# Performance work log

Hardware: AMD Instinct MI355X
Metric: run time of the kernel (lower is better)

The kernel has to match this reference:

```python
import jax, jax.numpy as jnp
import numpy as np

B, N, D, E, H = 16, 256, 64, 64, 8


def setup_inputs() -> dict:
    key = jax.random.key(0)
    ks = jax.random.split(key, 16)
    s = 0.05
    return {
        "query": jax.random.normal(ks[0], (B, N, D), jnp.float32),
        "edges_augmented": jax.random.normal(ks[1], (B, N, N, E), jnp.float32),
        "Wq": jax.random.normal(ks[2], (D, H * D), jnp.float32) * s,
        "bq": jnp.zeros((H * D,), jnp.float32),
        "Wk": jax.random.normal(ks[3], (D, H * D), jnp.float32) * s,
        "bk": jnp.zeros((H * D,), jnp.float32),
        "Wv": jax.random.normal(ks[4], (D, H * D), jnp.float32) * s,
        "bv": jnp.zeros((H * D,), jnp.float32),
        "Wa": jax.random.normal(ks[5], (E, H), jnp.float32) * s,
        "ba": jnp.zeros((H,), jnp.float32),
        "Wg": jax.random.normal(ks[6], (E, H), jnp.float32) * s,
        "bg": jnp.zeros((H,), jnp.float32),
        "Wo": jax.random.normal(ks[7], (H * D, D), jnp.float32) * s,
        "bo": jnp.zeros((D,), jnp.float32),
        "We": jax.random.normal(ks[8], (H, E), jnp.float32) * s,
        "be": jnp.zeros((E,), jnp.float32),
    }


def reference(query, edges_augmented, Wq, bq, Wk, bk, Wv, bv, Wa, ba, Wg, bg, Wo, bo, We, be):
    b, n, d = query.shape
    h = Wa.shape[1]
    # QKV projections -> [b, h, n, d]
    Q = (query @ Wq + bq).reshape(b, n, h, d).transpose(0, 2, 1, 3)
    Kt = (query @ Wk + bk).reshape(b, n, h, d).transpose(0, 2, 1, 3)
    V = (query @ Wv + bv).reshape(b, n, h, d).transpose(0, 2, 1, 3)
    scores = jnp.einsum('bhnd,bhmd->bhnm', Q, Kt) / jnp.sqrt(jnp.asarray(d, query.dtype))
    # edge-derived additive bias: [b,n,n,h] -> [b,h,n,n]
    attn_bias = (edges_augmented @ Wa + ba).transpose(0, 3, 1, 2)
    scores = scores + attn_bias
    # sigmoid gate on values
    g = jax.nn.sigmoid((edges_augmented @ Wg + bg).transpose(0, 3, 1, 2))  # [b,h,n,n]
    Vg = jnp.einsum('bhnm,bhmd->bhnd', g, V)
    attn = jax.nn.softmax(scores, axis=-1)
    out = jnp.einsum('bhnm,bhmd->bhnd', attn, Vg)
    out = out.transpose(0, 2, 1, 3).reshape(b, n, h * d)
    attention_output = out @ Wo + bo  # [b, n, d]
    # edges output: scores [b,h,n,m] -> [b,m,n,h] -> Dense to E
    edges_output = scores.transpose(0, 3, 2, 1) @ We + be  # [b, n, n, E]
    return (attention_output, edges_output)
```

## Files before the change

kernel.cpp:

```cpp
#include <hip/hip_runtime.h>

#define BB 16
#define NN 256
#define DD 64
#define EE 64
#define HH 8

typedef __attribute__((ext_vector_type(4))) float f32x4;
typedef __attribute__((ext_vector_type(8))) short short8;

__device__ __forceinline__ void fma4(float* acc, float x, float4 w) {
    acc[0] += x * w.x; acc[1] += x * w.y; acc[2] += x * w.z; acc[3] += x * w.w;
}

__device__ __forceinline__ unsigned short f2bf(float f) {
    union { float f; unsigned u; } v; v.f = f;
    unsigned r = v.u + 0x7FFFu + ((v.u >> 16) & 1u);
    return (unsigned short)(r >> 16);
}

__global__ __launch_bounds__(256) void qkv_kernel(
    const float* __restrict__ query,
    const float* __restrict__ Wq, const float* __restrict__ bq,
    const float* __restrict__ Wk, const float* __restrict__ bk,
    const float* __restrict__ Wv, const float* __restrict__ bv,
    unsigned short* __restrict__ Qb, unsigned short* __restrict__ Kb,
    unsigned short* __restrict__ Vtb)
{
    __shared__ __align__(16) float q_l[8][64];
    const int mtx = blockIdx.x >> 9;
    const int rem = blockIdx.x & 511;
    const int b   = rem >> 5;
    const int n0  = (rem & 31) << 3;
    const int tid = threadIdx.x;

    if (tid < 128)
        ((float4*)&q_l[0][0])[tid] =
            ((const float4*)(query + (size_t)(b * NN + n0) * DD))[tid];

    const int w    = tid >> 6;
    const int lane = tid & 63;
    const int r0   = w * 2;
    const float* W  = (mtx == 0) ? Wq : (mtx == 1) ? Wk : Wv;
    const float* bs = (mtx == 0) ? bq : (mtx == 1) ? bk : bv;

    const int c0 = lane << 2;
    float acc[2][2][4];
    {
        const float4 b0 = *(const float4*)(bs + c0);
        const float4 b1 = *(const float4*)(bs + 256 + c0);
        acc[0][0][0]=b0.x; acc[0][0][1]=b0.y; acc[0][0][2]=b0.z; acc[0][0][3]=b0.w;
        acc[0][1][0]=b1.x; acc[0][1][1]=b1.y; acc[0][1][2]=b1.z; acc[0][1][3]=b1.w;
        acc[1][0][0]=b0.x; acc[1][0][1]=b0.y; acc[1][0][2]=b0.z; acc[1][0][3]=b0.w;
        acc[1][1][0]=b1.x; acc[1][1][1]=b1.y; acc[1][1][2]=b1.z; acc[1][1][3]=b1.w;
    }
    __syncthreads();

    #pragma unroll 2
    for (int d4 = 0; d4 < 16; ++d4) {
        const float4 qa = ((const float4*)&q_l[r0][0])[d4];
        const float4 qb = ((const float4*)&q_l[r0 + 1][0])[d4];
        const float qav[4] = {qa.x, qa.y, qa.z, qa.w};
        const float qbv[4] = {qb.x, qb.y, qb.z, qb.w};
        #pragma unroll
        for (int k = 0; k < 4; ++k) {
            const float4 w0 = *(const float4*)(W + (size_t)(d4 * 4 + k) * 512 + c0);
            const float4 w1 = *(const float4*)(W + (size_t)(d4 * 4 + k) * 512 + 256 + c0);
            fma4(acc[0][0], qav[k], w0); fma4(acc[0][1], qav[k], w1);
            fma4(acc[1][0], qbv[k], w0); fma4(acc[1][1], qbv[k], w1);
        }
    }

    const int hq = lane >> 4;
    const int d0 = (lane & 15) << 2;
    if (mtx < 2) {
        unsigned short* T = (mtx == 0) ? Qb : Kb;
        const float scale = (mtx == 0) ? 0.125f : 1.0f;
        #pragma unroll
        for (int r = 0; r < 2; ++r)
            #pragma unroll
            for (int j = 0; j < 2; ++j) {
                const int h = j * 4 + hq;
                const unsigned int lo = (unsigned)f2bf(acc[r][j][0] * scale)
                                      | ((unsigned)f2bf(acc[r][j][1] * scale) << 16);
                const unsigned int hi = (unsigned)f2bf(acc[r][j][2] * scale)
                                      | ((unsigned)f2bf(acc[r][j][3] * scale) << 16);
                uint2* p = (uint2*)(T + ((size_t)(b * HH + h) * NN + n0 + r0 + r) * DD + d0);
                *p = make_uint2(lo, hi);
            }
    } else {
        #pragma unroll
        for (int r = 0; r < 2; ++r)
            #pragma unroll
            for (int j = 0; j < 2; ++j) {
                const int h = j * 4 + hq;
                #pragma unroll
                for (int k = 0; k < 4; ++k)
                    Vtb[((size_t)(b * HH + h) * DD + d0 + k) * NN + n0 + r0 + r] =
                        f2bf(acc[r][j][k]);
            }
    }
}

__global__ __launch_bounds__(256) void qk_kernel(
    const unsigned short* __restrict__ Qb, const unsigned short* __restrict__ Kb,
    float* __restrict__ scores)
{
    const int bh = blockIdx.x >> 3;
    const int nt = (blockIdx.x >> 1) & 3;
    const int mh = blockIdx.x & 1;
    const int tid = threadIdx.x;
    const int w = tid >> 6, l = tid & 63;
    const int lr = l & 15, lg = l >> 4;
    const int n0 = nt * 64 + w * 16;

    const unsigned short* qp = Qb + ((size_t)bh * NN + n0 + lr) * DD + lg * 8;
    const unsigned short* kp = Kb + ((size_t)bh * NN + mh * 128 + lr) * DD + lg * 8;

    const short8 a0 = *(const short8*)qp;
    const short8 a1 = *(const short8*)(qp + 32);

    f32x4 acc[8];
    #pragma unroll
    for (int mt = 0; mt < 8; ++mt) acc[mt] = (f32x4){0.f, 0.f, 0.f, 0.f};

    #pragma unroll
    for (int mt = 0; mt < 8; ++mt) {
        const short8 b0 = *(const short8*)(kp + (size_t)mt * 16 * DD);
        const short8 b1 = *(const short8*)(kp + (size_t)mt * 16 * DD + 32);
        acc[mt] = __builtin_amdgcn_mfma_f32_16x16x32_bf16(a0, b0, acc[mt], 0, 0, 0);
        acc[mt] = __builtin_amdgcn_mfma_f32_16x16x32_bf16(a1, b1, acc[mt], 0, 0, 0);
    }

    float* sp = scores + (size_t)bh * NN * NN;
    #pragma unroll
    for (int mt = 0; mt < 8; ++mt)
        #pragma unroll
        for (int r = 0; r < 4; ++r)
            sp[(size_t)(n0 + lg * 4 + r) * NN + mh * 128 + mt * 16 + lr] = acc[mt][r];
}

__global__ __launch_bounds__(256) void edges_kernel(
    const float* __restrict__ edges,
    const float* __restrict__ Wa, const float* __restrict__ ba,
    const float* __restrict__ Wg, const float* __restrict__ bg,
    const float* __restrict__ We, const float* __restrict__ be,
    float* __restrict__ scores,
    unsigned short* __restrict__ gates,
    float* __restrict__ edges_out)
{
    __shared__ __align__(16) float wa_l[EE * HH];
    __shared__ __align__(16) float wg_l[EE * HH];
    __shared__ float ba_l[HH], bg_l[HH];
    __shared__ __align__(16) float sc_l[4][64][HH];

    const int mt   = blockIdx.x & 3;
    const int nt   = (blockIdx.x >> 2) & 63;
    const int b    = blockIdx.x >> 8;
    const int n0   = nt << 2;
    const int m0   = mt << 6;
    const int tid  = threadIdx.x;
    const int lane = tid & 63;
    const int np   = tid >> 6;
    const int mp   = lane;

    for (int i = tid; i < 512; i += 256) { wa_l[i] = Wa[i]; wg_l[i] = Wg[i]; }
    if (tid < 8) { ba_l[tid] = ba[tid]; bg_l[tid] = bg[tid]; }

    float wecol[8];
    #pragma unroll
    for (int h = 0; h < 8; ++h) wecol[h] = We[h * EE + lane];
    const float bev = be[lane];

    const size_t so = (size_t)b * HH * NN * NN + (size_t)(n0 + np) * NN + m0 + mp;
    float qk[8];
    #pragma unroll
    for (int h = 0; h < 8; ++h) qk[h] = scores[so + (size_t)h * NN * NN];

    const float4* ep = (const float4*)(edges +
                        (size_t)((b * NN + n0 + np) * NN + m0 + mp) * DD);
    float4 xr[16];
    #pragma unroll
    for (int i = 0; i < 16; ++i) xr[i] = ep[i];

    __syncthreads();

    float bias[8], gate[8];
    #pragma unroll
    for (int h = 0; h < 8; ++h) { bias[h] = ba_l[h]; gate[h] = bg_l[h]; }
    #pragma unroll
    for (int e4 = 0; e4 < 16; ++e4) {
        const float xs[4] = {xr[e4].x, xr[e4].y, xr[e4].z, xr[e4].w};
        #pragma unroll
        for (int k = 0; k < 4; ++k) {
            const int e = e4 * 4 + k;
            const float4 wa0 = *(const float4*)&wa_l[e * 8];
            const float4 wa1 = *(const float4*)&wa_l[e * 8 + 4];
            const float4 wg0 = *(const float4*)&wg_l[e * 8];
            const float4 wg1 = *(const float4*)&wg_l[e * 8 + 4];
            fma4(&bias[0], xs[k], wa0); fma4(&bias[4], xs[k], wa1);
            fma4(&gate[0], xs[k], wg0); fma4(&gate[4], xs[k], wg1);
        }
    }

    float sc[8];
    #pragma unroll
    for (int h = 0; h < 8; ++h) {
        sc[h] = qk[h] + bias[h];
        const float gg = 1.f / (1.f + __expf(-gate[h]));
        scores[so + (size_t)h * NN * NN] = sc[h];
        gates [so + (size_t)h * NN * NN] = f2bf(gg);
    }
    *(float4*)&sc_l[np][mp][0] = make_float4(sc[0], sc[1], sc[2], sc[3]);
    *(float4*)&sc_l[np][mp][4] = make_float4(sc[4], sc[5], sc[6], sc[7]);
    __syncthreads();

    #pragma unroll 8
    for (int pi = 0; pi < 64; ++pi) {
        const int p   = np * 64 + pi;
        const int mp2 = p >> 2, np2 = p & 3;
        const float4 sa = *(const float4*)&sc_l[np2][mp2][0];
        const float4 sb = *(const float4*)&sc_l[np2][mp2][4];
        const float v = bev
            + sa.x * wecol[0] + sa.y * wecol[1] + sa.z * wecol[2] + sa.w * wecol[3]
            + sb.x * wecol[4] + sb.y * wecol[5] + sb.z * wecol[6] + sb.w * wecol[7];
        edges_out[(size_t)((b * NN + m0 + mp2) * NN + n0 + np2) * DD + lane] = v;
    }
}

__global__ __launch_bounds__(256) void vg_kernel(
    const unsigned short* __restrict__ gates, const unsigned short* __restrict__ Vtb,
    unsigned short* __restrict__ Vgt)
{
    const int bh = blockIdx.x >> 2;
    const int q  = blockIdx.x & 3;
    const int tid = threadIdx.x;
    const int w = tid >> 6, l = tid & 63;
    const int lr = l & 15, lg = l >> 4;
    const int n0 = q * 64 + w * 16;

    const unsigned short* gp = gates + ((size_t)bh * NN + n0 + lr) * NN + lg * 8;
    const unsigned short* vp = Vtb + ((size_t)bh * DD + lr) * NN + lg * 8;

    f32x4 acc[4];
    #pragma unroll
    for (int dt = 0; dt < 4; ++dt) acc[dt] = (f32x4){0.f, 0.f, 0.f, 0.f};

    #pragma unroll
    for (int ks = 0; ks < 8; ++ks) {
        const short8 bfr = *(const short8*)(gp + ks * 32);
        #pragma unroll
        for (int dt = 0; dt < 4; ++dt) {
            const short8 afr = *(const short8*)(vp + (size_t)dt * 16 * NN + ks * 32);
            acc[dt] = __builtin_amdgcn_mfma_f32_16x16x32_bf16(afr, bfr, acc[dt], 0, 0, 0);
        }
    }

    unsigned short* op = Vgt + (size_t)bh * DD * NN;
    #pragma unroll
    for (int dt = 0; dt < 4; ++dt)
        #pragma unroll
        for (int r = 0; r < 4; ++r)
            op[(size_t)(dt * 16 + lg * 4 + r) * NN + n0 + lr] = f2bf(acc[dt][r]);
}

__global__ __launch_bounds__(256) void out_kernel(
    const float* __restrict__ scores, const unsigned short* __restrict__ Vgt,
    const float* __restrict__ Wo, const float* __restrict__ bo,
    float* __restrict__ att_out)
{
    __shared__ __align__(16) float o_l[16][513];
    const int b  = blockIdx.x >> 4;
    const int nt = blockIdx.x & 15;
    const int n0 = nt * 16;
    const int tid = threadIdx.x;
    const int w = tid >> 6, l = tid & 63;
    const int lr = l & 15, lg = l >> 4;

    #pragma unroll
    for (int hw = 0; hw < 2; ++hw) {
        const int h = w + hw * 4;
        const float* sp = scores + ((size_t)(b * HH + h) * NN + n0 + lr) * NN + lg * 8;

        float s[64];
        #pragma unroll
        for (int ks = 0; ks < 8; ++ks) {
            const float4 x0 = *(const float4*)(sp + ks * 32);
            const float4 x1 = *(const float4*)(sp + ks * 32 + 4);
            s[ks * 8 + 0] = x0.x; s[ks * 8 + 1] = x0.y;
            s[ks * 8 + 2] = x0.z; s[ks * 8 + 3] = x0.w;
            s[ks * 8 + 4] = x1.x; s[ks * 8 + 5] = x1.y;
            s[ks * 8 + 6] = x1.z; s[ks * 8 + 7] = x1.w;
        }
        float mx = -1e30f;
        #pragma unroll
        for (int i = 0; i < 64; ++i) mx = fmaxf(mx, s[i]);
        mx = fmaxf(mx, __shfl_xor(mx, 16, 64));
        mx = fmaxf(mx, __shfl_xor(mx, 32, 64));
        float sm = 0.f;
        #pragma unroll
        for (int i = 0; i < 64; ++i) { s[i] = __expf(s[i] - mx); sm += s[i]; }
        sm += __shfl_xor(sm, 16, 64);
        sm += __shfl_xor(sm, 32, 64);
        const float inv = 1.f / sm;

        const unsigned short* vp = Vgt + ((size_t)(b * HH + h) * DD + lr) * NN + lg * 8;
        f32x4 acc[4];
        #pragma unroll
        for (int dt = 0; dt < 4; ++dt) acc[dt] = (f32x4){0.f, 0.f, 0.f, 0.f};

        #pragma unroll
        for (int ks = 0; ks < 8; ++ks) {
            union { short8 v; unsigned short u[8]; } bf;
            #pragma unroll
            for (int j = 0; j < 8; ++j) bf.u[j] = f2bf(s[ks * 8 + j] * inv);
            #pragma unroll
            for (int dt = 0; dt < 4; ++dt) {
                const short8 afr = *(const short8*)(vp + (size_t)dt * 16 * NN + ks * 32);
                acc[dt] = __builtin_amdgcn_mfma_f32_16x16x32_bf16(afr, bf.v, acc[dt], 0, 0, 0);
            }
        }
        #pragma unroll
        for (int dt = 0; dt < 4; ++dt)
            #pragma unroll
            for (int r = 0; r < 4; ++r)
                o_l[lr][h * 64 + dt * 16 + lg * 4 + r] = acc[dt][r];
    }
    __syncthreads();

    const int n  = tid >> 4;
    const int d4 = (tid & 15) << 2;
    float a0 = bo[d4], a1 = bo[d4 + 1], a2 = bo[d4 + 2], a3 = bo[d4 + 3];
    const float* orow = &o_l[n][0];
    #pragma unroll 8
    for (int k = 0; k < 512; ++k) {
        const float o = orow[k];
        const float4 w4 = *(const float4*)(Wo + (size_t)k * 64 + d4);
        a0 += o * w4.x; a1 += o * w4.y; a2 += o * w4.z; a3 += o * w4.w;
    }
    *(float4*)(att_out + ((size_t)(b * NN + n0 + n)) * DD + d4) =
        make_float4(a0, a1, a2, a3);
}

extern "C" void kernel_launch(void* const* d_in, const int* in_sizes, int n_in,
                              void* d_out, int out_size, void* d_ws, size_t ws_size,
                              hipStream_t stream)
{
    const float* query = (const float*)d_in[0];
    const float* edges = (const float*)d_in[1];
    const float* Wq = (const float*)d_in[2];  const float* bq = (const float*)d_in[3];
    const float* Wk = (const float*)d_in[4];  const float* bk = (const float*)d_in[5];
    const float* Wv = (const float*)d_in[6];  const float* bv = (const float*)d_in[7];
    const float* Wa = (const float*)d_in[8];  const float* ba = (const float*)d_in[9];
    const float* Wg = (const float*)d_in[10]; const float* bg = (const float*)d_in[11];
    const float* Wo = (const float*)d_in[12]; const float* bo = (const float*)d_in[13];
    const float* We = (const float*)d_in[14]; const float* be = (const float*)d_in[15];

    float* att_out   = (float*)d_out;
    float* edges_out = (float*)d_out + 262144;

    char* base = (char*)d_ws;
    float*          scores = (float*)base;
    unsigned short* gates  = (unsigned short*)(base + 33554432);
    unsigned short* Qb     = (unsigned short*)(base + 50331648);
    unsigned short* Kb     = (unsigned short*)(base + 54525952);
    unsigned short* Vtb    = (unsigned short*)(base + 58720256);
    unsigned short* Vgt    = (unsigned short*)(base + 62914560);

    hipLaunchKernelGGL(qkv_kernel, dim3(1536), dim3(256), 0, stream,
                       query, Wq, bq, Wk, bk, Wv, bv, Qb, Kb, Vtb);
    hipLaunchKernelGGL(qk_kernel, dim3(1024), dim3(256), 0, stream,
                       Qb, Kb, scores);
    hipLaunchKernelGGL(edges_kernel, dim3(4096), dim3(256), 0, stream,
                       edges, Wa, ba, Wg, bg, We, be, scores, gates, edges_out);
    hipLaunchKernelGGL(vg_kernel, dim3(512), dim3(256), 0, stream,
                       gates, Vtb, Vgt);
    hipLaunchKernelGGL(out_kernel, dim3(256), dim3(256), 0, stream,
                       scores, Vgt, Wo, bo, att_out);
}
```

Measured before the change: 601.6 us.

## Compute edge bias and gate projections with bf16 MFMA and restructure out kernel

The edges kernel now stages one row of 128 edge vectors per block in LDS as bf16, using an XOR-swizzled layout. It computes both the Wa and Wg projections with 16x16x32 bf16 MFMA instead of scalar FP32 FMAs. Each block now owns a single n row and half of the m range, so the grid doubles and the edges_out writes are organised per row. The out kernel moves from 256 to 512 threads, giving one wave per head instead of looping over two heads, and each thread handles two output columns. Converting the edges input to bf16 lowers the precision of the bias and gate values.

```diff
diff --git a/kernel.cpp b/kernel.cpp
--- a/kernel.cpp
+++ b/kernel.cpp
@@ -149,82 +149,91 @@
     unsigned short* __restrict__ gates,
     float* __restrict__ edges_out)
 {
-    __shared__ __align__(16) float wa_l[EE * HH];
-    __shared__ __align__(16) float wg_l[EE * HH];
-    __shared__ float ba_l[HH], bg_l[HH];
-    __shared__ __align__(16) float sc_l[4][64][HH];
-
-    const int mt   = blockIdx.x & 3;
-    const int nt   = (blockIdx.x >> 2) & 63;
-    const int b    = blockIdx.x >> 8;
-    const int n0   = nt << 2;
-    const int m0   = mt << 6;
-    const int tid  = threadIdx.x;
-    const int lane = tid & 63;
-    const int np   = tid >> 6;
-    const int mp   = lane;
-
-    for (int i = tid; i < 512; i += 256) { wa_l[i] = Wa[i]; wg_l[i] = Wg[i]; }
-    if (tid < 8) { ba_l[tid] = ba[tid]; bg_l[tid] = bg[tid]; }
+    __shared__ __align__(16) unsigned short eb[128 * 64];
+    __shared__ __align__(16) unsigned short wc[16 * 64];
+    __shared__ float bgl[128][17];
+    __shared__ float bal[8], bgb[8];
+
+    const int mh  = blockIdx.x & 1;
+    const int n   = (blockIdx.x >> 1) & 255;
+    const int b   = blockIdx.x >> 9;
+    const int m0  = mh << 7;
+    const int tid = threadIdx.x;
+    const int w   = tid >> 6, l = tid & 63;
+    const int lr  = l & 15, lg = l >> 4;
 
     float wecol[8];
     #pragma unroll
-    for (int h = 0; h < 8; ++h) wecol[h] = We[h * EE + lane];
-    const float bev = be[lane];
-
-    const size_t so = (size_t)b * HH * NN * NN + (size_t)(n0 + np) * NN + m0 + mp;
-    float qk[8];
-    #pragma unroll
-    for (int h = 0; h < 8; ++h) qk[h] = scores[so + (size_t)h * NN * NN];
-
-    const float4* ep = (const float4*)(edges +
-                        (size_t)((b * NN + n0 + np) * NN + m0 + mp) * DD);
-    float4 xr[16];
-    #pragma unroll
-    for (int i = 0; i < 16; ++i) xr[i] = ep[i];
-
-    __syncthreads();
-
-    float bias[8], gate[8];
-    #pragma unroll
-    for (int h = 0; h < 8; ++h) { bias[h] = ba_l[h]; gate[h] = bg_l[h]; }
-    #pragma unroll
-    for (int e4 = 0; e4 < 16; ++e4) {
-        const float xs[4] = {xr[e4].x, xr[e4].y, xr[e4].z, xr[e4].w};
-        #pragma unroll
-        for (int k = 0; k < 4; ++k) {
-            const int e = e4 * 4 + k;
-            const float4 wa0 = *(const float4*)&wa_l[e * 8];
-            const float4 wa1 = *(const float4*)&wa_l[e * 8 + 4];
-            const float4 wg0 = *(const float4*)&wg_l[e * 8];
-            const float4 wg1 = *(const float4*)&wg_l[e * 8 + 4];
-            fma4(&bias[0], xs[k], wa0); fma4(&bias[4], xs[k], wa1);
-            fma4(&gate[0], xs[k], wg0); fma4(&gate[4], xs[k], wg1);
-        }
-    }
-
-    float sc[8];
-    #pragma unroll
-    for (int h = 0; h < 8; ++h) {
-        sc[h] = qk[h] + bias[h];
-        const float gg = 1.f / (1.f + __expf(-gate[h]));
-        scores[so + (size_t)h * NN * NN] = sc[h];
-        gates [so + (size_t)h * NN * NN] = f2bf(gg);
-    }
-    *(float4*)&sc_l[np][mp][0] = make_float4(sc[0], sc[1], sc[2], sc[3]);
-    *(float4*)&sc_l[np][mp][4] = make_float4(sc[4], sc[5], sc[6], sc[7]);
-    __syncthreads();
-
-    #pragma unroll 8
-    for (int pi = 0; pi < 64; ++pi) {
-        const int p   = np * 64 + pi;
-        const int mp2 = p >> 2, np2 = p & 3;
-        const float4 sa = *(const float4*)&sc_l[np2][mp2][0];
-        const float4 sb = *(const float4*)&sc_l[np2][mp2][4];
-        const float v = bev
-            + sa.x * wecol[0] + sa.y * wecol[1] + sa.z * wecol[2] + sa.w * wecol[3]
-            + sb.x * wecol[4] + sb.y * wecol[5] + sb.z * wecol[6] + sb.w * wecol[7];
-        edges_out[(size_t)((b * NN + m0 + mp2) * NN + n0 + np2) * DD + lane] = v;
+    for (int h = 0; h < 8; ++h) wecol[h] = We[h * EE + l];
+    const float bev = be[l];
+
+    #pragma unroll
+    for (int j = 0; j < 4; ++j) {
+        const int idx = tid * 4 + j;
+        const int hp = idx >> 6, e = idx & 63;
+        const float v = (hp < 8) ? Wa[e * 8 + hp] : Wg[e * 8 + (hp - 8)];
+        *(unsigned short*)((char*)wc + hp * 128 + ((e * 2) ^ ((hp & 7) << 4))) = f2bf(v);
+    }
+    if (tid < 8) { bal[tid] = ba[tid]; bgb[tid] = bg[tid]; }
+
+    const float4* esrc = (const float4*)(edges + ((size_t)(b * NN + n) * NN + m0) * DD);
+    #pragma unroll
+    for (int it = 0; it < 8; ++it) {
+        const int c = it * 256 + tid;
+        const float4 x = esrc[c];
+        const int m = c >> 4, e4 = c & 15;
+        const unsigned lo = (unsigned)f2bf(x.x) | ((unsigned)f2bf(x.y) << 16);
+        const unsigned hi = (unsigned)f2bf(x.z) | ((unsigned)f2bf(x.w) << 16);
+        *(uint2*)((char*)eb + m * 128 + ((e4 * 8) ^ ((m & 7) << 4))) = make_uint2(lo, hi);
+    }
+    __syncthreads();
+
+    short8 bfrag[2];
+    #pragma unroll
+    for (int ks = 0; ks < 2; ++ks)
+        bfrag[ks] = *(const short8*)((char*)wc + lr * 128 +
+                                     ((ks * 64 + lg * 16) ^ ((lr & 7) << 4)));
+
+    #pragma unroll
+    for (int t = 0; t < 2; ++t) {
+        const int T = w * 2 + t;
+        f32x4 acc = (f32x4){0.f, 0.f, 0.f, 0.f};
+        #pragma unroll
+        for (int ks = 0; ks < 2; ++ks) {
+            const int m = T * 16 + lr;
+            const short8 af = *(const short8*)((char*)eb + m * 128 +
+                                 ((ks * 64 + lg * 16) ^ ((lr & 7) << 4)));
+            acc = __builtin_amdgcn_mfma_f32_16x16x32_bf16(af, bfrag[ks], acc, 0, 0, 0);
+        }
+        #pragma unroll
+        for (int r = 0; r < 4; ++r)
+            bgl[T * 16 + lg * 4 + r][lr] = acc[r];
+    }
+    __syncthreads();
+
+    {
+        const int m  = tid & 127;
+        const int hh = tid >> 7;
+        #pragma unroll
+        for (int i = 0; i < 4; ++i) {
+            const int h = hh * 4 + i;
+            const size_t off = ((size_t)(b * HH + h) << 16) + (n << 8) + m0 + m;
+            const float sc = scores[off] + bgl[m][h] + bal[h];
+            scores[off] = sc;
+            bgl[m][h]   = sc;
+            const float gv = bgl[m][8 + h] + bgb[h];
+            gates[off] = f2bf(1.f / (1.f + __expf(-gv)));
+        }
+    }
+    __syncthreads();
+
+    #pragma unroll 4
+    for (int mi = 0; mi < 32; ++mi) {
+        const int m = w * 32 + mi;
+        float v = bev;
+        #pragma unroll
+        for (int h = 0; h < 8; ++h) v += bgl[m][h] * wecol[h];
+        edges_out[((size_t)(b * NN + m0 + m) * NN + n) * DD + l] = v;
     }
 }
 
@@ -264,24 +273,22 @@
             op[(size_t)(dt * 16 + lg * 4 + r) * NN + n0 + lr] = f2bf(acc[dt][r]);
 }
 
-__global__ __launch_bounds__(256) void out_kernel(
+__global__ __launch_bounds__(512) void out_kernel(
     const float* __restrict__ scores, const unsigned short* __restrict__ Vgt,
     const float* __restrict__ Wo, const float* __restrict__ bo,
     float* __restrict__ att_out)
 {
-    __shared__ __align__(16) float o_l[16][513];
+    __shared__ float o_l[16][521];
     const int b  = blockIdx.x >> 4;
     const int nt = blockIdx.x & 15;
     const int n0 = nt * 16;
     const int tid = threadIdx.x;
     const int w = tid >> 6, l = tid & 63;
     const int lr = l & 15, lg = l >> 4;
-
-    #pragma unroll
-    for (int hw = 0; hw < 2; ++hw) {
-        const int h = w + hw * 4;
+    const int h = w;
+
+    {
         const float* sp = scores + ((size_t)(b * HH + h) * NN + n0 + lr) * NN + lg * 8;
-
         float s[64];
         #pragma unroll
         for (int ks = 0; ks < 8; ++ks) {
@@ -328,18 +335,17 @@
     }
     __syncthreads();
 
-    const int n  = tid >> 4;
-    const int d4 = (tid & 15) << 2;
-    float a0 = bo[d4], a1 = bo[d4 + 1], a2 = bo[d4 + 2], a3 = bo[d4 + 3];
+    const int n  = tid >> 5;
+    const int d2 = (tid & 31) << 1;
+    float a0 = bo[d2], a1 = bo[d2 + 1];
     const float* orow = &o_l[n][0];
     #pragma unroll 8
     for (int k = 0; k < 512; ++k) {
         const float o = orow[k];
-        const float4 w4 = *(const float4*)(Wo + (size_t)k * 64 + d4);
-        a0 += o * w4.x; a1 += o * w4.y; a2 += o * w4.z; a3 += o * w4.w;
-    }
-    *(float4*)(att_out + ((size_t)(b * NN + n0 + n)) * DD + d4) =
-        make_float4(a0, a1, a2, a3);
+        const float2 w2 = *(const float2*)(Wo + (size_t)k * 64 + d2);
+        a0 += o * w2.x; a1 += o * w2.y;
+    }
+    *(float2*)(att_out + ((size_t)(b * NN + n0 + n)) * DD + d2) = make_float2(a0, a1);
 }
 
 extern "C" void kernel_launch(void* const* d_in, const int* in_sizes, int n_in,
@@ -371,10 +377,10 @@
                        query, Wq, bq, Wk, bk, Wv, bv, Qb, Kb, Vtb);
     hipLaunchKernelGGL(qk_kernel, dim3(1024), dim3(256), 0, stream,
                        Qb, Kb, scores);
-    hipLaunchKernelGGL(edges_kernel, dim3(4096), dim3(256), 0, stream,
+    hipLaunchKernelGGL(edges_kernel, dim3(8192), dim3(256), 0, stream,
                        edges, Wa, ba, Wg, bg, We, be, scores, gates, edges_out);
     hipLaunchKernelGGL(vg_kernel, dim3(512), dim3(256), 0, stream,
                        gates, Vtb, Vgt);
-    hipLaunchKernelGGL(out_kernel, dim3(256), dim3(256), 0, stream,
+    hipLaunchKernelGGL(out_kernel, dim3(256), dim3(512), 0, stream,
                        scores, Vgt, Wo, bo, att_out);
 }
```

After: 588.8 us. 2.1% less time.
